# Optimization experiments

Hardware: AMD Instinct MI355X
Metric: run time of the kernel (lower is better)

## Reference

```python
import jax, jax.numpy as jnp
import numpy as np

B, T, E, H, V = 32, 120, 300, 256, 32000
C, G = 512, 7

def setup_inputs() -> dict:
    key = jax.random.key(0)
    ks = jax.random.split(key, 8)
    s = lambda k, shape, sc: (jax.random.normal(k, shape, jnp.float32) * sc)
    return {
        "features": jax.random.normal(ks[0], (B, C, G, G), jnp.float32),
        "embeddings": jax.random.normal(ks[1], (B, T, E), jnp.float32),
        "W_init": s(ks[2], (H, C), 0.04),          # nn.Linear(512, num_layers*H)
        "b_init": jnp.zeros((H,), jnp.float32),
        "W_fc2": s(ks[3], (H, C * G * G), 0.006),   # nn.Linear(512*49, H)
        "b_fc2": jnp.zeros((H,), jnp.float32),
        "W_ih": s(ks[4], (3 * H, E + H), 0.04),     # GRU weight_ih_l0 (r,z,n rows)
        "b_ih": jnp.zeros((3 * H,), jnp.float32),
        "W_hh": s(ks[5], (3 * H, H), 0.06),         # GRU weight_hh_l0
        "b_hh": jnp.zeros((3 * H,), jnp.float32),
        "W_fc": s(ks[6], (V, H), 0.06),             # nn.Linear(H, vocab)
        "b_fc": jnp.zeros((V,), jnp.float32),
        "length": T,
    }

def reference(features, embeddings, W_init, b_init, W_fc2, b_fc2,
              W_ih, b_ih, W_hh, b_hh, W_fc, b_fc, length):
    Bq, Cq = features.shape[0], features.shape[1]
    Hq = W_hh.shape[1]
    # init_hidden_state: [B,C,7,7] -> [B,49,C]
    f = jnp.transpose(features, (0, 2, 3, 1)).reshape(Bq, -1, Cq)
    h0 = f.mean(axis=1) @ W_init.T + b_init                      # [B,H], num_layers=1
    # flatten + fc2, broadcast over time, concat with embeddings
    feat = f.reshape(Bq, -1) @ W_fc2.T + b_fc2                   # [B,H]
    x = jnp.concatenate(
        [embeddings,
         jnp.broadcast_to(feat[:, None, :], (Bq, embeddings.shape[1], Hq))],
        axis=-1)                                                  # [B,T,E+H]
    xs = jnp.transpose(x[:, :length], (1, 0, 2))                  # [T,B,E+H]
    # precompute input-side gate projections for all timesteps (one big GEMM)
    gi = jnp.einsum('tbi,gi->tbg', xs, W_ih) + b_ih               # [T,B,3H]
    def step(h, g_x):
        g_h = h @ W_hh.T + b_hh
        r = jax.nn.sigmoid(g_x[..., :Hq] + g_h[..., :Hq])
        z = jax.nn.sigmoid(g_x[..., Hq:2 * Hq] + g_h[..., Hq:2 * Hq])
        n = jnp.tanh(g_x[..., 2 * Hq:] + r * g_h[..., 2 * Hq:])
        h_new = (1.0 - z) * n + z * h
        return h_new, h_new
    _, hs = jax.lax.scan(step, h0, gi)                            # [T,B,H]
    # per-step fc (dropout p=0.3 is identity in eval mode)
    logits = jnp.einsum('tbh,vh->btv', hs, W_fc) + b_fc           # [B,T,V]
    return logits
```

## Files before the change

### kernel.cpp

```cpp
#include <hip/hip_runtime.h>
#include <hip/hip_bf16.h>

#define BB 32
#define TT 120
#define EE 300
#define HH 256
#define VV 32000
#define CC 512
#define GG 49
#define KIN 556
#define CF 25088

typedef __attribute__((ext_vector_type(8))) short bf16x8;
typedef __attribute__((ext_vector_type(4))) float f32x4;

__device__ __forceinline__ float bpair_lo(unsigned int u) { return __uint_as_float(u << 16); }
__device__ __forceinline__ float bpair_hi(unsigned int u) { return __uint_as_float(u & 0xFFFF0000u); }

__device__ __forceinline__ unsigned int packbf(float a, float b) {
    union { __hip_bfloat16 h; unsigned short u; } ua, ub;
    ua.h = __float2bfloat16(a); ub.h = __float2bfloat16(b);
    return (unsigned int)ua.u | ((unsigned int)ub.u << 16);
}

#if defined(__has_builtin)
#  if __has_builtin(__builtin_amdgcn_fdot2_f32_bf16)
#    define USE_DOT2 1
#  endif
#endif
#ifndef USE_DOT2
#  define USE_DOT2 0
#endif

#if USE_DOT2
typedef __bf16 bf2_t __attribute__((ext_vector_type(2)));
__device__ __forceinline__ float dot2bf(unsigned int w, unsigned int h, float c) {
    return __builtin_amdgcn_fdot2_f32_bf16(__builtin_bit_cast(bf2_t, w),
                                           __builtin_bit_cast(bf2_t, h), c, false);
}
#else
__device__ __forceinline__ float dot2bf(unsigned int w, unsigned int h, float c) {
    c = fmaf(bpair_lo(w), bpair_lo(h), c);
    c = fmaf(bpair_hi(w), bpair_hi(h), c);
    return c;
}
#endif

__global__ void __launch_bounds__(256) k_pre(const float* __restrict__ features,
                                             const float* __restrict__ W_fc2,
                                             float* __restrict__ part,
                                             const float* __restrict__ W_hh,
                                             unsigned int* __restrict__ whh_bf,
                                             const float* __restrict__ W_init,
                                             const float* __restrict__ b_init,
                                             float* __restrict__ h0) {
    __shared__ float xs[98][BB];
    __shared__ float mf[CC];
    __shared__ float red[8][33];
    int bid = blockIdx.x;
    if (bid < 256) {
        int kc = bid;
        for (int idx = threadIdx.x; idx < 98 * BB; idx += 256) {
            int ii = idx >> 5, b = idx & 31;
            int ig = kc * 98 + ii;
            int c = ig & 511, p = ig >> 9;
            xs[ii][b] = features[(size_t)b * CF + c * GG + p];
        }
        __syncthreads();
        int h = threadIdx.x;
        float acc[BB];
#pragma unroll
        for (int b = 0; b < BB; ++b) acc[b] = 0.f;
        const float* wp = W_fc2 + (size_t)h * CF + kc * 98;
        for (int ii = 0; ii < 98; ii += 2) {
            float2 w2 = *(const float2*)(wp + ii);
            const float4* x0 = (const float4*)&xs[ii][0];
            const float4* x1 = (const float4*)&xs[ii + 1][0];
#pragma unroll
            for (int q = 0; q < 8; ++q) {
                float4 a4 = x0[q], b4 = x1[q];
                acc[4 * q + 0] += w2.x * a4.x + w2.y * b4.x;
                acc[4 * q + 1] += w2.x * a4.y + w2.y * b4.y;
                acc[4 * q + 2] += w2.x * a4.z + w2.y * b4.z;
                acc[4 * q + 3] += w2.x * a4.w + w2.y * b4.w;
            }
        }
        float* pp = part + (size_t)kc * (BB * 256) + h;
#pragma unroll
        for (int b = 0; b < BB; ++b) pp[b * 256] = acc[b];
    } else if (bid < 640) {
        int idx = (bid - 256) * 256 + threadIdx.x;
        float2 w2 = *(const float2*)(W_hh + (size_t)idx * 2);
        whh_bf[idx] = packbf(w2.x, w2.y);
    } else {
        int lb = bid - 640;
        int b  = lb >> 3;
        int hc = lb & 7;
        {
            const float* p = features + (size_t)b * CF + (size_t)threadIdx.x * 2 * GG;
            float s0 = 0.f, s1 = 0.f;
#pragma unroll
            for (int i = 0; i < GG; ++i) s0 += p[i];
#pragma unroll
            for (int i = 0; i < GG; ++i) s1 += p[GG + i];
            mf[threadIdx.x * 2]     = s0 * (1.0f / 49.0f);
            mf[threadIdx.x * 2 + 1] = s1 * (1.0f / 49.0f);
        }
        __syncthreads();
        int h  = threadIdx.x & 31;
        int kg = threadIdx.x >> 5;
        int gh = hc * 32 + h;
        const float* w = W_init + (size_t)gh * CC + kg * 64;
        const float* m = mf + kg * 64;
        float s = 0.f;
#pragma unroll
        for (int k = 0; k < 64; k += 4) {
            float4 w4 = *(const float4*)(w + k);
            s += m[k] * w4.x + m[k + 1] * w4.y + m[k + 2] * w4.z + m[k + 3] * w4.w;
        }
        red[kg][h] = s;
        __syncthreads();
        if (threadIdx.x < 32) {
            float t = b_init[hc * 32 + threadIdx.x];
#pragma unroll
            for (int g = 0; g < 8; ++g) t += red[g][threadIdx.x];
            h0[b * HH + hc * 32 + threadIdx.x] = t;
        }
    }
}

__global__ void __launch_bounds__(256) k_fc2b(const float* __restrict__ part,
                                              const float* __restrict__ b_fc2,
                                              float* __restrict__ feat) {
    int b  = blockIdx.x;
    int hc = blockIdx.y;
    int h  = threadIdx.x & 31;
    int kg = threadIdx.x >> 5;
    int gh = hc * 32 + h;
    __shared__ float red[8][33];
    const float* pp = part + (size_t)kg * 32 * (BB * 256) + b * 256 + gh;
    float s = 0.f;
#pragma unroll
    for (int kc = 0; kc < 32; ++kc) s += pp[(size_t)kc * (BB * 256)];
    red[kg][h] = s;
    __syncthreads();
    if (threadIdx.x < 32) {
        float t = b_fc2[hc * 32 + threadIdx.x];
#pragma unroll
        for (int g = 0; g < 8; ++g) t += red[g][threadIdx.x];
        feat[b * HH + hc * 32 + threadIdx.x] = t;
    }
}

__global__ void __launch_bounds__(256) k_gi(const float* __restrict__ emb,
                                            const float* __restrict__ feat,
                                            const float* __restrict__ W_ih,
                                            const float* __restrict__ b_ih,
                                            float* __restrict__ gi) {
    __shared__ float As[64][68];
    __shared__ float Bs[64][68];
    int n0 = blockIdx.x * 64;
    int m0 = blockIdx.y * 64;
    int tid = threadIdx.x;
    int tm = (tid & 15) * 4;
    int tn = (tid >> 4) * 4;
    float acc[4][4] = {};

    int mrA[4], klA[4];
#pragma unroll
    for (int s = 0; s < 4; ++s) {
        int slot = tid * 4 + s;
        mrA[s] = slot >> 4;
        klA[s] = (slot & 15) * 4;
    }

    float4 ra[4], rb[4];

#define LOADG(KC)                                                                 \
    do {                                                                          \
        int k0_ = (KC) * 64;                                                      \
        _Pragma("unroll") for (int s = 0; s < 4; ++s) {                           \
            int m = m0 + mrA[s];                                                  \
            int t = m >> 5, b = m & 31;                                           \
            int kg = k0_ + klA[s];                                                \
            if (kg + 4 <= EE) {                                                   \
                ra[s] = *(const float4*)(emb + ((size_t)b * TT + t) * EE + kg);   \
            } else if (kg >= EE && kg + 4 <= KIN) {                               \
                ra[s] = *(const float4*)(feat + (size_t)b * HH + (kg - EE));      \
            } else {                                                              \
                float tmp[4];                                                     \
                _Pragma("unroll") for (int q = 0; q < 4; ++q) {                   \
                    int kq = kg + q;                                              \
                    tmp[q] = (kq < EE) ? emb[((size_t)b * TT + t) * EE + kq]      \
                           : (kq < KIN) ? feat[(size_t)b * HH + (kq - EE)] : 0.f; \
                }                                                                 \
                ra[s] = *(float4*)tmp;                                            \
            }                                                                     \
        }                                                                         \
        _Pragma("unroll") for (int s = 0; s < 4; ++s) {                           \
            int gidx = n0 + mrA[s];                                               \
            int kg = k0_ + klA[s];                                                \
            if (kg + 4 <= KIN) {                                                  \
                rb[s] = *(const float4*)(W_ih + (size_t)gidx * KIN + kg);         \
            } else {                                                              \
                float tmp[4];                                                     \
                _Pragma("unroll") for (int q = 0; q < 4; ++q) {                   \
                    int kq = kg + q;                                              \
                    tmp[q] = (kq < KIN) ? W_ih[(size_t)gidx * KIN + kq] : 0.f;    \
                }                                                                 \
                rb[s] = *(float4*)tmp;                                            \
            }                                                                     \
        }                                                                         \
    } while (0)

#define STORES()                                                                  \
    do {                                                                          \
        _Pragma("unroll") for (int s = 0; s < 4; ++s) {                           \
            As[klA[s] + 0][mrA[s]] = ra[s].x;                                     \
            As[klA[s] + 1][mrA[s]] = ra[s].y;                                     \
            As[klA[s] + 2][mrA[s]] = ra[s].z;                                     \
            As[klA[s] + 3][mrA[s]] = ra[s].w;                                     \
            Bs[klA[s] + 0][mrA[s]] = rb[s].x;                                     \
            Bs[klA[s] + 1][mrA[s]] = rb[s].y;                                     \
            Bs[klA[s] + 2][mrA[s]] = rb[s].z;                                     \
            Bs[klA[s] + 3][mrA[s]] = rb[s].w;                                     \
        }                                                                         \
    } while (0)

    LOADG(0);
#pragma unroll 1
    for (int kc = 0; kc < 9; ++kc) {
        __syncthreads();
        STORES();
        if (kc < 8) LOADG(kc + 1);
        __syncthreads();
        int kmax = (kc == 8) ? 44 : 64;
        for (int k = 0; k < kmax; ++k) {
            float4 av = *(const float4*)&As[k][tm];
            float4 bv = *(const float4*)&Bs[k][tn];
            const float* ap = (const float*)&av;
            const float* bp = (const float*)&bv;
#pragma unroll
            for (int i = 0; i < 4; ++i)
#pragma unroll
                for (int j = 0; j < 4; ++j)
                    acc[i][j] = fmaf(ap[i], bp[j], acc[i][j]);
        }
    }
#undef LOADG
#undef STORES

    float4 bias = *(const float4*)(b_ih + n0 + tn);
    const float* bp = (const float*)&bias;
#pragma unroll
    for (int i = 0; i < 4; ++i) {
        int m = m0 + tm + i;
        float4 o;
        o.x = acc[i][0] + bp[0];
        o.y = acc[i][1] + bp[1];
        o.z = acc[i][2] + bp[2];
        o.w = acc[i][3] + bp[3];
        *(float4*)(gi + (size_t)m * 768 + n0 + tn) = o;
    }
}

__device__ __forceinline__ void gru_body(int b, const float* __restrict__ h0,
                                         const float* __restrict__ gi,
                                         const unsigned int* __restrict__ whh_bf,
                                         const float* __restrict__ b_hh,
                                         __hip_bfloat16* __restrict__ hA,
                                         unsigned int* h_pk, float* hf,
                                         float* r_sh, float* z_sh) {
    int jp = threadIdx.x;
    int j  = jp & 255;
    int g  = jp >> 8;
    const unsigned int* wr = whh_bf + (size_t)jp * 128;
    float bias = b_hh[jp];
    if (jp < HH) hf[jp] = h0[b * HH + jp];
    __syncthreads();
    if (jp < 128) h_pk[jp] = packbf(hf[2 * jp], hf[2 * jp + 1]);
    __syncthreads();

    for (int t = 0; t < TT; ++t) {
        float a0 = 0.f, a1 = 0.f, a2 = 0.f, a3 = 0.f;
#pragma unroll
        for (int kk = 0; kk < 128; kk += 4) {
            uint4 wq = *(const uint4*)(wr + kk);
            uint4 hq = *(const uint4*)&h_pk[kk];
            a0 = dot2bf(wq.x, hq.x, a0);
            a1 = dot2bf(wq.y, hq.y, a1);
            a2 = dot2bf(wq.z, hq.z, a2);
            a3 = dot2bf(wq.w, hq.w, a3);
        }
        float a = (a0 + a1) + (a2 + a3);
        float gx = gi[((size_t)t * BB + b) * 768 + jp];
        if (g == 0)      r_sh[j] = 1.f / (1.f + __expf(-(gx + a + bias)));
        else if (g == 1) z_sh[j] = 1.f / (1.f + __expf(-(gx + a + bias)));
        __syncthreads();
        if (g == 2) {
            float n  = tanhf(gx + r_sh[j] * (a + bias));
            float z  = z_sh[j];
            float hn = (1.f - z) * n + z * hf[j];
            hf[j] = hn;
            hA[((size_t)b * TT + t) * HH + j] = __float2bfloat16(hn);
        }
        __syncthreads();
        if (jp < 128) h_pk[jp] = packbf(hf[2 * jp], hf[2 * jp + 1]);
        __syncthreads();
    }
}

__global__ void __launch_bounds__(768, 3) k_gru(const float* __restrict__ h0,
                                                const float* __restrict__ gi,
                                                const unsigned int* __restrict__ whh_bf,
                                                const float* __restrict__ b_hh,
                                                __hip_bfloat16* __restrict__ hA) {
    __shared__ unsigned int h_pk[128];
    __shared__ float hf[256];
    __shared__ float r_sh[256];
    __shared__ float z_sh[256];
    gru_body(blockIdx.x, h0, gi, whh_bf, b_hh, hA, h_pk, hf, r_sh, z_sh);
}

#define CVT_N4 2048000
__global__ void __launch_bounds__(768, 3) k_gru_cvt(const float* __restrict__ h0,
                                                    const float* __restrict__ gi,
                                                    const unsigned int* __restrict__ whh_bf,
                                                    const float* __restrict__ b_hh,
                                                    __hip_bfloat16* __restrict__ hA,
                                                    const float* __restrict__ W_fc,
                                                    __hip_bfloat16* __restrict__ wfc) {
    if (blockIdx.x >= 32) {
        size_t base = (size_t)(blockIdx.x - 32) * (768 * 4) + threadIdx.x;
#pragma unroll
        for (int q = 0; q < 4; ++q) {
            size_t fi = base + (size_t)q * 768;
            if (fi < CVT_N4) {
                float4 v = *((const float4*)W_fc + fi);
                __hip_bfloat16 o[4];
                o[0] = __float2bfloat16(v.x);
                o[1] = __float2bfloat16(v.y);
                o[2] = __float2bfloat16(v.z);
                o[3] = __float2bfloat16(v.w);
                *((uint2*)wfc + fi) = *(uint2*)o;
            }
        }
        return;
    }
    __shared__ unsigned int h_pk[128];
    __shared__ float hf[256];
    __shared__ float r_sh[256];
    __shared__ float z_sh[256];
    gru_body(blockIdx.x, h0, gi, whh_bf, b_hh, hA, h_pk, hf, r_sh, z_sh);
}

__global__ void k_cvt(const float* __restrict__ src, __hip_bfloat16* __restrict__ dst) {
    size_t i = ((size_t)blockIdx.x * 256 + threadIdx.x) * 4;
    float4 v = *(const float4*)(src + i);
    __hip_bfloat16 o[4];
    o[0] = __float2bfloat16(v.x);
    o[1] = __float2bfloat16(v.y);
    o[2] = __float2bfloat16(v.z);
    o[3] = __float2bfloat16(v.w);
    *(uint2*)(dst + i) = *(uint2*)o;
}

__global__ void __launch_bounds__(256) k_logits(const __hip_bfloat16* __restrict__ hA,
                                                const __hip_bfloat16* __restrict__ wfc,
                                                const float* __restrict__ b_fc,
                                                float* __restrict__ out) {
    __shared__ __align__(16) short smemAB[2][128][64];
    char* AsB = (char*)smemAB[0];
    char* BsB = (char*)smemAB[1];
    float* eb = (float*)smemAB;

    int nt = blockIdx.x;
    int mt = blockIdx.y;
    int tid  = threadIdx.x;
    int wave = tid >> 6, lane = tid & 63;
    int wm = wave >> 1, wn = wave & 1;
    int lr = lane & 15;
    int lk = lane >> 4;

    int rs = tid >> 3;
    int cs = tid & 7;
    const short* Ag = (const short*)hA  + (size_t)mt * 128 * HH + (size_t)rs * HH + cs * 8;
    const short* Bg = (const short*)wfc + (size_t)nt * 128 * HH + (size_t)rs * HH + cs * 8;
    int wswz = (cs ^ (rs & 7)) * 16;
    int wofs[4];
#pragma unroll
    for (int p = 0; p < 4; ++p) wofs[p] = (p * 32 + rs) * 128 + wswz;

    f32x4 acc[4][4] = {};

#define LOADT(kt, GA, GB)                                                        \
    do {                                                                         \
        _Pragma("unroll") for (int p = 0; p < 4; ++p)                            \
            GA[p] = *(const bf16x8*)(Ag + (size_t)p * 32 * HH + (kt) * 64);      \
        _Pragma("unroll") for (int p = 0; p < 4; ++p)                            \
            GB[p] = *(const bf16x8*)(Bg + (size_t)p * 32 * HH + (kt) * 64);      \
    } while (0)

#define STORET(GA, GB)                                                           \
    do {                                                                         \
        _Pragma("unroll") for (int p = 0; p < 4; ++p)                            \
            *(bf16x8*)(AsB + wofs[p]) = GA[p];                                   \
        _Pragma("unroll") for (int p = 0; p < 4; ++p)                            \
            *(bf16x8*)(BsB + wofs[p]) = GB[p];                                   \
    } while (0)

#define COMPUTE()                                                                \
    do {                                                                         \
        _Pragma("unroll") for (int kk = 0; kk < 2; ++kk) {                       \
            bf16x8 af[4], bg[4];                                                 \
            _Pragma("unroll") for (int i = 0; i < 4; ++i) {                      \
                int r = wm * 64 + i * 16 + lr;                                   \
                af[i] = *(const bf16x8*)(AsB + r * 128 + (((kk * 4 + lk) ^ (r & 7)) * 16)); \
            }                                                                    \
            _Pragma("unroll") for (int j = 0; j < 4; ++j) {                      \
                int r = wn * 64 + j * 16 + lr;                                   \
                bg[j] = *(const bf16x8*)(BsB + r * 128 + (((kk * 4 + lk) ^ (r & 7)) * 16)); \
            }                                                                    \
            _Pragma("unroll") for (int i = 0; i < 4; ++i)                        \
                _Pragma("unroll") for (int j = 0; j < 4; ++j)                    \
                    acc[i][j] = __builtin_amdgcn_mfma_f32_16x16x32_bf16(af[i], bg[j], acc[i][j], 0, 0, 0); \
        }                                                                        \
    } while (0)

    bf16x8 gA[4], gB[4], gA2[4], gB2[4];
    LOADT(0, gA, gB);
    STORET(gA, gB);   LOADT(1, gA2, gB2); __syncthreads(); COMPUTE(); __syncthreads();
    STORET(gA2, gB2); LOADT(2, gA, gB);   __syncthreads(); COMPUTE(); __syncthreads();
    STORET(gA, gB);   LOADT(3, gA2, gB2); __syncthreads(); COMPUTE(); __syncthreads();
    STORET(gA2, gB2);                     __syncthreads(); COMPUTE();

#undef LOADT
#undef STORET
#undef COMPUTE

    int mloc = wm * 64;
#pragma unroll 1
    for (int nh = 0; nh < 2; ++nh) {
        __syncthreads();
        if (wn == nh) {
#pragma unroll
            for (int j = 0; j < 4; ++j) {
                int v = nt * 128 + nh * 64 + j * 16 + lr;
                float bias = b_fc[v];
#pragma unroll
                for (int i = 0; i < 4; ++i) {
#pragma unroll
                    for (int q = 0; q < 4; ++q)
                        eb[(mloc + i * 16 + lk * 4 + q) * 64 + j * 16 + lr] = acc[i][j][q] + bias;
                }
            }
        }
        __syncthreads();
        size_t obase = (size_t)(mt * 128) * VV + nt * 128 + nh * 64;
#pragma unroll
        for (int pass = 0; pass < 8; ++pass) {
            int idx = pass * 256 + tid;
            int row = idx >> 4;
            int c4 = (idx & 15) * 4;
            float4 vv = *(const float4*)&eb[row * 64 + c4];
            *(float4*)(out + obase + (size_t)row * VV + c4) = vv;
        }
    }
}

extern "C" void kernel_launch(void* const* d_in, const int* in_sizes, int n_in,
                              void* d_out, int out_size, void* d_ws, size_t ws_size,
                              hipStream_t stream) {
    (void)in_sizes; (void)n_in; (void)out_size;
    const float* features   = (const float*)d_in[0];
    const float* embeddings = (const float*)d_in[1];
    const float* W_init     = (const float*)d_in[2];
    const float* b_init     = (const float*)d_in[3];
    const float* W_fc2      = (const float*)d_in[4];
    const float* b_fc2      = (const float*)d_in[5];
    const float* W_ih       = (const float*)d_in[6];
    const float* b_ih       = (const float*)d_in[7];
    const float* W_hh       = (const float*)d_in[8];
    const float* b_hh       = (const float*)d_in[9];
    const float* W_fc       = (const float*)d_in[10];
    const float* b_fc       = (const float*)d_in[11];

    char* ws = (char*)d_ws;
    float* feat   = (float*)(ws + 65536);
    float* hbuf0  = (float*)(ws + 98304);
    __hip_bfloat16* hA = (__hip_bfloat16*)(ws + 131072);
    float* gi     = (float*)(ws + 2097152);
    float* part   = (float*)(ws + 2097152);
    unsigned int* whh_bf = (unsigned int*)(ws + 13893632);
    float* outp = (float*)d_out;

    int fused = (ws_size >= 30670848u);
    __hip_bfloat16* wfc = fused ? (__hip_bfloat16*)(ws + 14286848)
                                : (__hip_bfloat16*)(ws + 2097152);

    k_pre<<<896, 256, 0, stream>>>(features, W_fc2, part, W_hh, whh_bf, W_init, b_init, hbuf0);
    k_fc2b<<<dim3(32, 8), 256, 0, stream>>>(part, b_fc2, feat);
    k_gi<<<dim3(12, 60), 256, 0, stream>>>(embeddings, feat, W_ih, b_ih, gi);
    if (fused) {
        k_gru_cvt<<<32 + 667, 768, 0, stream>>>(hbuf0, gi, whh_bf, b_hh, hA, W_fc, wfc);
    } else {
        k_gru<<<32, 768, 0, stream>>>(hbuf0, gi, whh_bf, b_hh, hA);
        k_cvt<<<8000, 256, 0, stream>>>(W_fc, wfc);
    }
    k_logits<<<dim3(250, 30), 256, 0, stream>>>(hA, wfc, b_fc, outp);
}
```

Before: 431.0 us.

## Enlarge logits GEMM tile to 256x128 with 512 threads and store directly

```diff
diff --git a/kernel.cpp b/kernel.cpp
--- a/kernel.cpp
+++ b/kernel.cpp
@@ -365,48 +365,56 @@
     *(uint2*)(dst + i) = *(uint2*)o;
 }
 
-__global__ void __launch_bounds__(256) k_logits(const __hip_bfloat16* __restrict__ hA,
+__global__ void __launch_bounds__(512) k_logits(const __hip_bfloat16* __restrict__ hA,
                                                 const __hip_bfloat16* __restrict__ wfc,
                                                 const float* __restrict__ b_fc,
                                                 float* __restrict__ out) {
-    __shared__ __align__(16) short smemAB[2][128][64];
-    char* AsB = (char*)smemAB[0];
-    char* BsB = (char*)smemAB[1];
-    float* eb = (float*)smemAB;
+    __shared__ short As[256][64];
+    __shared__ short Bs[128][64];
+    char* AsB = (char*)As;
+    char* BsB = (char*)Bs;
 
     int nt = blockIdx.x;
     int mt = blockIdx.y;
     int tid  = threadIdx.x;
     int wave = tid >> 6, lane = tid & 63;
-    int wm = wave >> 1, wn = wave & 1;
+    int wm = wave >> 1;
+    int wn = wave & 1;
     int lr = lane & 15;
     int lk = lane >> 4;
 
     int rs = tid >> 3;
     int cs = tid & 7;
-    const short* Ag = (const short*)hA  + (size_t)mt * 128 * HH + (size_t)rs * HH + cs * 8;
-    const short* Bg = (const short*)wfc + (size_t)nt * 128 * HH + (size_t)rs * HH + cs * 8;
-    int wswz = (cs ^ (rs & 7)) * 16;
-    int wofs[4];
-#pragma unroll
-    for (int p = 0; p < 4; ++p) wofs[p] = (p * 32 + rs) * 128 + wswz;
+    const short* Ag = (const short*)hA  + ((size_t)mt * 256 + rs) * HH + cs * 8;
+    const short* Bg = (const short*)wfc + ((size_t)nt * 128 + rs) * HH + cs * 8;
+    int wofsA[4], wofsB[2];
+#pragma unroll
+    for (int s = 0; s < 4; ++s) {
+        int row = s * 64 + rs;
+        wofsA[s] = row * 128 + ((cs ^ (row & 7)) * 16);
+    }
+#pragma unroll
+    for (int s = 0; s < 2; ++s) {
+        int row = s * 64 + rs;
+        wofsB[s] = row * 128 + ((cs ^ (row & 7)) * 16);
+    }
 
     f32x4 acc[4][4] = {};
 
 #define LOADT(kt, GA, GB)                                                        \
     do {                                                                         \
-        _Pragma("unroll") for (int p = 0; p < 4; ++p)                            \
-            GA[p] = *(const bf16x8*)(Ag + (size_t)p * 32 * HH + (kt) * 64);      \
-        _Pragma("unroll") for (int p = 0; p < 4; ++p)                            \
-            GB[p] = *(const bf16x8*)(Bg + (size_t)p * 32 * HH + (kt) * 64);      \
+        _Pragma("unroll") for (int s = 0; s < 4; ++s)                            \
+            GA[s] = *(const bf16x8*)(Ag + (size_t)s * 64 * HH + (kt) * 64);      \
+        _Pragma("unroll") for (int s = 0; s < 2; ++s)                            \
+            GB[s] = *(const bf16x8*)(Bg + (size_t)s * 64 * HH + (kt) * 64);      \
     } while (0)
 
 #define STORET(GA, GB)                                                           \
     do {                                                                         \
-        _Pragma("unroll") for (int p = 0; p < 4; ++p)                            \
-            *(bf16x8*)(AsB + wofs[p]) = GA[p];                                   \
-        _Pragma("unroll") for (int p = 0; p < 4; ++p)                            \
-            *(bf16x8*)(BsB + wofs[p]) = GB[p];                                   \
+        _Pragma("unroll") for (int s = 0; s < 4; ++s)                            \
+            *(bf16x8*)(AsB + wofsA[s]) = GA[s];                                  \
+        _Pragma("unroll") for (int s = 0; s < 2; ++s)                            \
+            *(bf16x8*)(BsB + wofsB[s]) = GB[s];                                  \
     } while (0)
 
 #define COMPUTE()                                                                \
@@ -427,7 +435,7 @@
         }                                                                        \
     } while (0)
 
-    bf16x8 gA[4], gB[4], gA2[4], gB2[4];
+    bf16x8 gA[4], gB[2], gA2[4], gB2[2];
     LOADT(0, gA, gB);
     STORET(gA, gB);   LOADT(1, gA2, gB2); __syncthreads(); COMPUTE(); __syncthreads();
     STORET(gA2, gB2); LOADT(2, gA, gB);   __syncthreads(); COMPUTE(); __syncthreads();
@@ -438,32 +446,19 @@
 #undef STORET
 #undef COMPUTE
 
-    int mloc = wm * 64;
-#pragma unroll 1
-    for (int nh = 0; nh < 2; ++nh) {
-        __syncthreads();
-        if (wn == nh) {
-#pragma unroll
-            for (int j = 0; j < 4; ++j) {
-                int v = nt * 128 + nh * 64 + j * 16 + lr;
-                float bias = b_fc[v];
-#pragma unroll
-                for (int i = 0; i < 4; ++i) {
-#pragma unroll
-                    for (int q = 0; q < 4; ++q)
-                        eb[(mloc + i * 16 + lk * 4 + q) * 64 + j * 16 + lr] = acc[i][j][q] + bias;
-                }
+    int m_base = mt * 256 + wm * 64;
+    int n_base = nt * 128 + wn * 64;
+#pragma unroll
+    for (int i = 0; i < 4; ++i) {
+#pragma unroll
+        for (int j = 0; j < 4; ++j) {
+            int v = n_base + j * 16 + lr;
+            float bias = b_fc[v];
+#pragma unroll
+            for (int q = 0; q < 4; ++q) {
+                int m = m_base + i * 16 + lk * 4 + q;
+                out[(size_t)m * VV + v] = acc[i][j][q] + bias;
             }
-        }
-        __syncthreads();
-        size_t obase = (size_t)(mt * 128) * VV + nt * 128 + nh * 64;
-#pragma unroll
-        for (int pass = 0; pass < 8; ++pass) {
-            int idx = pass * 256 + tid;
-            int row = idx >> 4;
-            int c4 = (idx & 15) * 4;
-            float4 vv = *(const float4*)&eb[row * 64 + c4];
-            *(float4*)(out + obase + (size_t)row * VV + c4) = vv;
         }
     }
 }
@@ -507,5 +502,5 @@
         k_gru<<<32, 768, 0, stream>>>(hbuf0, gi, whh_bf, b_hh, hA);
         k_cvt<<<8000, 256, 0, stream>>>(W_fc, wfc);
     }
-    k_logits<<<dim3(250, 30), 256, 0, stream>>>(hA, wfc, b_fc, outp);
-}
+    k_logits<<<dim3(250, 15), 512, 0, stream>>>(hA, wfc, b_fc, outp);
+}
```

New measurement: 400.0 us. -7.2%, faster.
